# Performance work log

Measured on AMD Instinct MI355X. Metric: run time of the kernel, lower is better.

## Reference

```python
import jax, jax.numpy as jnp
import numpy as np

N_NODES = 50000
N_EDGES = 500000
H_FEATS = 128
N_TYPES = 8

def setup_inputs() -> dict:
    key = jax.random.key(0)
    ks = jax.random.split(key, 7)
    h = jax.random.normal(ks[0], (N_NODES, H_FEATS), dtype=jnp.float32)
    src = jax.random.randint(ks[1], (N_EDGES,), 0, N_NODES, dtype=jnp.int64)
    dst = jax.random.randint(ks[2], (N_EDGES,), 0, N_NODES, dtype=jnp.int64)
    # nn.Linear default init scale ~ 1/sqrt(fan_in); plain normals scaled for sanity
    W1 = jax.random.normal(ks[3], (H_FEATS, 2 * H_FEATS), dtype=jnp.float32) / np.sqrt(2 * H_FEATS)
    b1 = jax.random.normal(ks[4], (H_FEATS,), dtype=jnp.float32) * 0.01
    W2 = jax.random.normal(ks[5], (N_TYPES, H_FEATS), dtype=jnp.float32) / np.sqrt(H_FEATS)
    b2 = jax.random.normal(ks[6], (N_TYPES,), dtype=jnp.float32) * 0.01
    return {"h": h, "src": src, "dst": dst, "W1": W1, "b1": b1, "W2": W2, "b2": b2}

def reference(h, src, dst, W1, b1, W2, b2):
    # Per-edge gather of src/dst node features, concat along feature dim: [E, 2H]
    e = jnp.concatenate([h[src], h[dst]], axis=1)
    # 2-layer MLP (torch Linear: x @ W.T + b), then softmax over edge-type logits
    hidden = jax.nn.relu(e @ W1.T + b1)            # [E, H]
    logits = hidden @ W2.T + b2                    # [E, T]
    return jax.nn.softmax(logits, axis=1)          # [E, T]; torch .squeeze(1) is a no-op for T>1
```

## Files before the change

kernel.cpp:

```cpp
#include <hip/hip_runtime.h>
#include <cstdint>
#include <cstddef>

#define HF 128
#define NTY 8

typedef __attribute__((ext_vector_type(8))) short short8;
typedef __attribute__((ext_vector_type(8))) _Float16 half8;
typedef __attribute__((ext_vector_type(4))) float f32x4;
typedef unsigned int u32;
typedef unsigned short u16;

__device__ __forceinline__ short f2bf(float x) {
  union { float f; unsigned u; } v; v.f = x;
  unsigned r = v.u + 0x7FFFu + ((v.u >> 16) & 1u);
  return (short)(r >> 16);
}
__device__ __forceinline__ float bf2f(short b) {
  union { unsigned u; float f; } v; v.u = ((unsigned)(unsigned short)b) << 16;
  return v.f;
}
__device__ __forceinline__ u16 f2h(float x) {
  union { _Float16 h; u16 u; } v; v.h = (_Float16)x; return v.u;
}
__device__ __forceinline__ u32 pk_addrelu_f16(u32 p, u32 q) {
  u32 r;
  asm("v_pk_add_f16 %0, %1, %2" : "=v"(r) : "v"(p), "v"(q));
  asm("v_pk_max_f16 %0, %1, 0"  : "=v"(r) : "v"(r));
  return r;
}

__global__ __launch_bounds__(256, 1) void node_pq_mfma(
    const float* __restrict__ h, const float* __restrict__ W1,
    const float* __restrict__ b1, u16* __restrict__ PQ,
    int n_nodes, int n_tiles)
{
  __shared__ short Bs[256 * HF];
  __shared__ short As[2][64 * HF];
  const int t    = threadIdx.x;
  const int lane = t & 63;
  const int w    = t >> 6;
  const int cl   = lane & 15;
  const int kg   = lane >> 4;

  {
    const int j = t;
    const float* src = (j < HF) ? (W1 + (size_t)j * 256)
                                : (W1 + (size_t)(j - HF) * 256 + HF);
#pragma unroll
    for (int c = 0; c < 16; ++c) {
      const float4 x = *(const float4*)(src + 8 * c);
      const float4 y = *(const float4*)(src + 8 * c + 4);
      short8 b;
      b[0]=f2bf(x.x); b[1]=f2bf(x.y); b[2]=f2bf(x.z); b[3]=f2bf(x.w);
      b[4]=f2bf(y.x); b[5]=f2bf(y.y); b[6]=f2bf(y.z); b[7]=f2bf(y.w);
      *(short8*)(&Bs[j * HF + ((c ^ (j & 7)) << 3)]) = b;
    }
  }

  const int ar = t >> 2;
  const int aq = t & 3;
  float4 pf[8];

  auto loadA = [&](int tile) {
    int node = tile * 64 + ar;
    if (node >= n_nodes) node = n_nodes - 1;
    const float* p = h + (size_t)node * HF + 32 * aq;
#pragma unroll
    for (int i = 0; i < 8; ++i) pf[i] = *(const float4*)(p + 4 * i);
  };
  auto writeA = [&]() {
#pragma unroll
    for (int ci = 0; ci < 4; ++ci) {
      const int c = 4 * aq + ci;
      const float4 x = pf[2 * ci], y = pf[2 * ci + 1];
      float f[8] = {x.x, x.y, x.z, x.w, y.x, y.y, y.z, y.w};
      short8 hi, lo;
#pragma unroll
      for (int i = 0; i < 8; ++i) {
        const short hb = f2bf(f[i]);
        hi[i] = hb;
        lo[i] = f2bf(f[i] - bf2f(hb));
      }
      const int off = ar * HF + ((c ^ (ar & 7)) << 3);
      *(short8*)(&As[0][off]) = hi;
      *(short8*)(&As[1][off]) = lo;
    }
  };

  float bias[4];
#pragma unroll
  for (int ni = 0; ni < 4; ++ni) {
    const int j = 64 * w + 16 * ni + cl;
    bias[ni] = (j < HF) ? b1[j] : 0.0f;
  }

  int tile = blockIdx.x;
  if (tile < n_tiles) { loadA(tile); writeA(); }
  __syncthreads();

  for (; tile < n_tiles; tile += gridDim.x) {
    int nxt = tile + gridDim.x;
    if (nxt >= n_tiles) nxt = tile;
    loadA(nxt);

    f32x4 acc[4][4];
#pragma unroll
    for (int mi = 0; mi < 4; ++mi)
#pragma unroll
      for (int ni = 0; ni < 4; ++ni)
        acc[mi][ni] = f32x4{bias[ni], bias[ni], bias[ni], bias[ni]};

#pragma unroll
    for (int ks = 0; ks < 4; ++ks) {
      const int kc = ks * 4 + kg;
      short8 ah[4], al[4], bb[4];
#pragma unroll
      for (int mi = 0; mi < 4; ++mi) {
        const int r = 16 * mi + cl;
        const int off = r * HF + ((kc ^ (r & 7)) << 3);
        ah[mi] = *(const short8*)(&As[0][off]);
        al[mi] = *(const short8*)(&As[1][off]);
      }
#pragma unroll
      for (int ni = 0; ni < 4; ++ni) {
        const int j = 64 * w + 16 * ni + cl;
        bb[ni] = *(const short8*)(&Bs[j * HF + ((kc ^ (j & 7)) << 3)]);
      }
#pragma unroll
      for (int mi = 0; mi < 4; ++mi)
#pragma unroll
        for (int ni = 0; ni < 4; ++ni) {
          acc[mi][ni] = __builtin_amdgcn_mfma_f32_16x16x32_bf16(ah[mi], bb[ni], acc[mi][ni], 0, 0, 0);
          acc[mi][ni] = __builtin_amdgcn_mfma_f32_16x16x32_bf16(al[mi], bb[ni], acc[mi][ni], 0, 0, 0);
        }
    }

#pragma unroll
    for (int mi = 0; mi < 4; ++mi) {
      const int rb = tile * 64 + 16 * mi + 4 * kg;
#pragma unroll
      for (int ni = 0; ni < 4; ++ni) {
        const int j = 64 * w + 16 * ni + cl;
#pragma unroll
        for (int reg = 0; reg < 4; ++reg) {
          const int node = rb + reg;
          if (node < n_nodes)
            PQ[(size_t)node * 256 + j] = f2h(acc[mi][ni][reg]);
        }
      }
    }

    __syncthreads();
    writeA();
    __syncthreads();
  }
}

__global__ __launch_bounds__(256) void edge_mlp_mfma(
    const u16* __restrict__ PQ, const int* __restrict__ src,
    const int* __restrict__ dst, const float* __restrict__ W2,
    const float* __restrict__ b2, float* __restrict__ out, int n_edges)
{
  const int t    = threadIdx.x;
  const int lane = t & 63;
  const int cl   = lane & 15;
  const int kg   = lane >> 4;

  half8 bf[4];
#pragma unroll
  for (int ks = 0; ks < 4; ++ks) {
    if (cl < NTY) {
      const float* wp = W2 + cl * HF + 32 * ks + 8 * kg;
      const float4 x = *(const float4*)wp;
      const float4 y = *(const float4*)(wp + 4);
      bf[ks][0]=(_Float16)x.x; bf[ks][1]=(_Float16)x.y;
      bf[ks][2]=(_Float16)x.z; bf[ks][3]=(_Float16)x.w;
      bf[ks][4]=(_Float16)y.x; bf[ks][5]=(_Float16)y.y;
      bf[ks][6]=(_Float16)y.z; bf[ks][7]=(_Float16)y.w;
    } else {
#pragma unroll
      for (int i = 0; i < 8; ++i) bf[ks][i] = (_Float16)0.0f;
    }
  }
  const float bbias = (cl < NTY) ? b2[cl] : 0.0f;

  const int gw = blockIdx.x * 4 + (t >> 6);
  const int nw = gridDim.x * 4;

  for (int base = gw * 16; base < n_edges; base += nw * 16) {
    int e = base + cl;
    if (e >= n_edges) e = n_edges - 1;
    const int s = src[e];
    const int d = dst[e];
    const u16* pr = PQ + (size_t)s * 256 + 8 * kg;
    const u16* qr = PQ + (size_t)d * 256 + HF + 8 * kg;

    uint4 P[4], Q[4];
#pragma unroll
    for (int ks = 0; ks < 4; ++ks) P[ks] = *(const uint4*)(pr + 32 * ks);
#pragma unroll
    for (int ks = 0; ks < 4; ++ks) Q[ks] = *(const uint4*)(qr + 32 * ks);

    f32x4 acc = f32x4{0.0f, 0.0f, 0.0f, 0.0f};
#pragma unroll
    for (int ks = 0; ks < 4; ++ks) {
      union { u32 w[4]; half8 v; } a;
      a.w[0] = pk_addrelu_f16(P[ks].x, Q[ks].x);
      a.w[1] = pk_addrelu_f16(P[ks].y, Q[ks].y);
      a.w[2] = pk_addrelu_f16(P[ks].z, Q[ks].z);
      a.w[3] = pk_addrelu_f16(P[ks].w, Q[ks].w);
      acc = __builtin_amdgcn_mfma_f32_16x16x32_f16(a.v, bf[ks], acc, 0, 0, 0);
    }

    float val[4];
#pragma unroll
    for (int r = 0; r < 4; ++r) {
      const float L = acc[r] + bbias;
      float m = fmaxf(L, __shfl_xor(L, 1, 64));
      m = fmaxf(m, __shfl_xor(m, 2, 64));
      m = fmaxf(m, __shfl_xor(m, 4, 64));
      const float ex = __expf(L - m);
      float sm = ex + __shfl_xor(ex, 1, 64);
      sm += __shfl_xor(sm, 2, 64);
      sm += __shfl_xor(sm, 4, 64);
      val[r] = ex / sm;
    }

    if (cl < NTY) {
#pragma unroll
      for (int r = 0; r < 4; ++r) {
        const int ee = base + 4 * kg + r;
        if (ee < n_edges) out[(size_t)ee * NTY + cl] = val[r];
      }
    }
  }
}

extern "C" void kernel_launch(void* const* d_in, const int* in_sizes, int n_in,
                              void* d_out, int out_size, void* d_ws, size_t ws_size,
                              hipStream_t stream) {
  const float* h   = (const float*)d_in[0];
  const int*   src = (const int*)d_in[1];
  const int*   dst = (const int*)d_in[2];
  const float* W1  = (const float*)d_in[3];
  const float* b1  = (const float*)d_in[4];
  const float* W2  = (const float*)d_in[5];
  const float* b2  = (const float*)d_in[6];
  float* out = (float*)d_out;

  const int n_nodes = in_sizes[0] / HF;
  const int n_edges = in_sizes[1];
  u16* PQ = (u16*)d_ws;

  const int n_tiles = (n_nodes + 63) / 64;
  hipLaunchKernelGGL(node_pq_mfma, dim3(256), dim3(256), 0, stream,
                     h, W1, b1, PQ, n_nodes, n_tiles);
  hipLaunchKernelGGL(edge_mlp_mfma, dim3(2048), dim3(256), 0, stream,
                     PQ, src, dst, W2, b2, out, n_edges);
}
```

Measured before the change: 71.79 us.

## Restructure node projection: pre-convert W1 to bf16, register-resident h tiles, no LDS

```diff
diff --git a/kernel.cpp b/kernel.cpp
--- a/kernel.cpp
+++ b/kernel.cpp
@@ -16,12 +16,16 @@
   unsigned r = v.u + 0x7FFFu + ((v.u >> 16) & 1u);
   return (short)(r >> 16);
 }
-__device__ __forceinline__ float bf2f(short b) {
-  union { unsigned u; float f; } v; v.u = ((unsigned)(unsigned short)b) << 16;
-  return v.f;
-}
 __device__ __forceinline__ u16 f2h(float x) {
   union { _Float16 h; u16 u; } v; v.h = (_Float16)x; return v.u;
+}
+__device__ __forceinline__ float asf(u32 u) {
+  union { u32 x; float f; } v; v.x = u; return v.f;
+}
+__device__ __forceinline__ u32 cvtpk_bf16(float a, float b) {
+  u32 r;
+  asm("v_cvt_pk_bf16_f32 %0, %1, %2" : "=v"(r) : "v"(a), "v"(b));
+  return r;
 }
 __device__ __forceinline__ u32 pk_addrelu_f16(u32 p, u32 q) {
   u32 r;
@@ -30,130 +34,77 @@
   return r;
 }
 
-__global__ __launch_bounds__(256, 1) void node_pq_mfma(
-    const float* __restrict__ h, const float* __restrict__ W1,
-    const float* __restrict__ b1, u16* __restrict__ PQ,
-    int n_nodes, int n_tiles)
+__global__ __launch_bounds__(256) void prep_w(
+    const float* __restrict__ W1, u16* __restrict__ Wbf)
 {
-  __shared__ short Bs[256 * HF];
-  __shared__ short As[2][64 * HF];
+  const int id = blockIdx.x * 256 + threadIdx.x;
+  const int j = id >> 4, c = id & 15;
+  const float* src = W1 + (size_t)(j & 127) * 256 + ((j >> 7) << 7) + 8 * c;
+  const float4 x = *(const float4*)src;
+  const float4 y = *(const float4*)(src + 4);
+  short8 b;
+  b[0]=f2bf(x.x); b[1]=f2bf(x.y); b[2]=f2bf(x.z); b[3]=f2bf(x.w);
+  b[4]=f2bf(y.x); b[5]=f2bf(y.y); b[6]=f2bf(y.z); b[7]=f2bf(y.w);
+  *(short8*)(&Wbf[(size_t)j * HF + 8 * c]) = b;
+}
+
+__global__ __launch_bounds__(512) void node_pq_v2(
+    const float* __restrict__ h, const u16* __restrict__ Wbf,
+    const float* __restrict__ b1, u16* __restrict__ PQ, int n_nodes)
+{
   const int t    = threadIdx.x;
   const int lane = t & 63;
-  const int w    = t >> 6;
+  const int wid  = t >> 6;
+  const int wq   = wid & 3;
+  const int wsb  = wid >> 2;
   const int cl   = lane & 15;
   const int kg   = lane >> 4;
-
-  {
-    const int j = t;
-    const float* src = (j < HF) ? (W1 + (size_t)j * 256)
-                                : (W1 + (size_t)(j - HF) * 256 + HF);
-#pragma unroll
-    for (int c = 0; c < 16; ++c) {
-      const float4 x = *(const float4*)(src + 8 * c);
-      const float4 y = *(const float4*)(src + 8 * c + 4);
-      short8 b;
-      b[0]=f2bf(x.x); b[1]=f2bf(x.y); b[2]=f2bf(x.z); b[3]=f2bf(x.w);
-      b[4]=f2bf(y.x); b[5]=f2bf(y.y); b[6]=f2bf(y.z); b[7]=f2bf(y.w);
-      *(short8*)(&Bs[j * HF + ((c ^ (j & 7)) << 3)]) = b;
-    }
-  }
-
-  const int ar = t >> 2;
-  const int aq = t & 3;
-  float4 pf[8];
-
-  auto loadA = [&](int tile) {
-    int node = tile * 64 + ar;
-    if (node >= n_nodes) node = n_nodes - 1;
-    const float* p = h + (size_t)node * HF + 32 * aq;
-#pragma unroll
-    for (int i = 0; i < 8; ++i) pf[i] = *(const float4*)(p + 4 * i);
-  };
-  auto writeA = [&]() {
-#pragma unroll
-    for (int ci = 0; ci < 4; ++ci) {
-      const int c = 4 * aq + ci;
-      const float4 x = pf[2 * ci], y = pf[2 * ci + 1];
-      float f[8] = {x.x, x.y, x.z, x.w, y.x, y.y, y.z, y.w};
-      short8 hi, lo;
-#pragma unroll
-      for (int i = 0; i < 8; ++i) {
-        const short hb = f2bf(f[i]);
-        hi[i] = hb;
-        lo[i] = f2bf(f[i] - bf2f(hb));
-      }
-      const int off = ar * HF + ((c ^ (ar & 7)) << 3);
-      *(short8*)(&As[0][off]) = hi;
-      *(short8*)(&As[1][off]) = lo;
-    }
-  };
-
-  float bias[4];
-#pragma unroll
-  for (int ni = 0; ni < 4; ++ni) {
-    const int j = 64 * w + 16 * ni + cl;
-    bias[ni] = (j < HF) ? b1[j] : 0.0f;
-  }
-
-  int tile = blockIdx.x;
-  if (tile < n_tiles) { loadA(tile); writeA(); }
-  __syncthreads();
-
-  for (; tile < n_tiles; tile += gridDim.x) {
-    int nxt = tile + gridDim.x;
-    if (nxt >= n_tiles) nxt = tile;
-    loadA(nxt);
-
-    f32x4 acc[4][4];
-#pragma unroll
-    for (int mi = 0; mi < 4; ++mi)
-#pragma unroll
-      for (int ni = 0; ni < 4; ++ni)
-        acc[mi][ni] = f32x4{bias[ni], bias[ni], bias[ni], bias[ni]};
-
+  const int nodeR = blockIdx.x * 32 + 16 * wsb + cl;
+  const int node  = (nodeR < n_nodes) ? nodeR : (n_nodes - 1);
+
+  const float* hp = h + (size_t)node * HF;
+  short8 bh[4], bl[4];
+#pragma unroll
+  for (int ks = 0; ks < 4; ++ks) {
+    const float4 x = *(const float4*)(hp + 32 * ks + 8 * kg);
+    const float4 y = *(const float4*)(hp + 32 * ks + 8 * kg + 4);
+    const float f[8] = {x.x, x.y, x.z, x.w, y.x, y.y, y.z, y.w};
+    union { u32 w[4]; short8 v; } H, L;
+#pragma unroll
+    for (int p = 0; p < 4; ++p) {
+      const float a = f[2 * p], b = f[2 * p + 1];
+      const u32 hb = cvtpk_bf16(a, b);
+      const float ea = a - asf(hb << 16);
+      const float eb = b - asf(hb & 0xFFFF0000u);
+      H.w[p] = hb;
+      L.w[p] = cvtpk_bf16(ea, eb);
+    }
+    bh[ks] = H.v;
+    bl[ks] = L.v;
+  }
+
+#pragma unroll
+  for (int mi = 0; mi < 4; ++mi) {
+    const int j0 = 64 * wq + 16 * mi;
+    f32x4 acc;
+    if (wq < 2) {
+      const float4 bv = *(const float4*)(b1 + j0 + 4 * kg);
+      acc = f32x4{bv.x, bv.y, bv.z, bv.w};
+    } else {
+      acc = f32x4{0.0f, 0.0f, 0.0f, 0.0f};
+    }
 #pragma unroll
     for (int ks = 0; ks < 4; ++ks) {
-      const int kc = ks * 4 + kg;
-      short8 ah[4], al[4], bb[4];
-#pragma unroll
-      for (int mi = 0; mi < 4; ++mi) {
-        const int r = 16 * mi + cl;
-        const int off = r * HF + ((kc ^ (r & 7)) << 3);
-        ah[mi] = *(const short8*)(&As[0][off]);
-        al[mi] = *(const short8*)(&As[1][off]);
-      }
-#pragma unroll
-      for (int ni = 0; ni < 4; ++ni) {
-        const int j = 64 * w + 16 * ni + cl;
-        bb[ni] = *(const short8*)(&Bs[j * HF + ((kc ^ (j & 7)) << 3)]);
-      }
-#pragma unroll
-      for (int mi = 0; mi < 4; ++mi)
-#pragma unroll
-        for (int ni = 0; ni < 4; ++ni) {
-          acc[mi][ni] = __builtin_amdgcn_mfma_f32_16x16x32_bf16(ah[mi], bb[ni], acc[mi][ni], 0, 0, 0);
-          acc[mi][ni] = __builtin_amdgcn_mfma_f32_16x16x32_bf16(al[mi], bb[ni], acc[mi][ni], 0, 0, 0);
-        }
-    }
-
-#pragma unroll
-    for (int mi = 0; mi < 4; ++mi) {
-      const int rb = tile * 64 + 16 * mi + 4 * kg;
-#pragma unroll
-      for (int ni = 0; ni < 4; ++ni) {
-        const int j = 64 * w + 16 * ni + cl;
-#pragma unroll
-        for (int reg = 0; reg < 4; ++reg) {
-          const int node = rb + reg;
-          if (node < n_nodes)
-            PQ[(size_t)node * 256 + j] = f2h(acc[mi][ni][reg]);
-        }
-      }
-    }
-
-    __syncthreads();
-    writeA();
-    __syncthreads();
+      const short8 af = *(const short8*)(Wbf + (size_t)(j0 + cl) * HF + 32 * ks + 8 * kg);
+      acc = __builtin_amdgcn_mfma_f32_16x16x32_bf16(af, bh[ks], acc, 0, 0, 0);
+      acc = __builtin_amdgcn_mfma_f32_16x16x32_bf16(af, bl[ks], acc, 0, 0, 0);
+    }
+    if (nodeR < n_nodes) {
+      uint2 o;
+      o.x = (u32)f2h(acc[0]) | ((u32)f2h(acc[1]) << 16);
+      o.y = (u32)f2h(acc[2]) | ((u32)f2h(acc[3]) << 16);
+      *(uint2*)(&PQ[(size_t)nodeR * 256 + j0 + 4 * kg]) = o;
+    }
   }
 }
 
@@ -251,11 +202,12 @@
 
   const int n_nodes = in_sizes[0] / HF;
   const int n_edges = in_sizes[1];
-  u16* PQ = (u16*)d_ws;
-
-  const int n_tiles = (n_nodes + 63) / 64;
-  hipLaunchKernelGGL(node_pq_mfma, dim3(256), dim3(256), 0, stream,
-                     h, W1, b1, PQ, n_nodes, n_tiles);
+  u16* PQ  = (u16*)d_ws;
+  u16* Wbf = PQ + (size_t)n_nodes * 256;
+
+  hipLaunchKernelGGL(prep_w, dim3(16), dim3(256), 0, stream, W1, Wbf);
+  hipLaunchKernelGGL(node_pq_v2, dim3((n_nodes + 31) / 32), dim3(512), 0, stream,
+                     h, Wbf, b1, PQ, n_nodes);
   hipLaunchKernelGGL(edge_mlp_mfma, dim3(2048), dim3(256), 0, stream,
                      PQ, src, dst, W2, b2, out, n_edges);
 }
```

Measured after the change: 94.13 us. 31.1% more time.
